# Optimization experiments

Hardware: AMD Instinct MI355X
Metric: run time of the kernel (lower is better)

Reference implementation:

```python
import jax, jax.numpy as jnp
import numpy as np

IN_F, H, T, NUM_CLASSES, WINDOW_HALF = 14, 24, 25, 4, 12


def _lstm_dir(x_tbf, w_ih, w_hh, b_ih, b_hh, reverse):
    # x_tbf: [T,B,F]; w_ih: [4H,F]; w_hh: [4H,H]; biases: [4H]
    B = x_tbf.shape[1]
    xw = jnp.einsum('tbf,gf->tbg', x_tbf, w_ih) + b_ih + b_hh  # [T,B,4H]

    def step(carry, xw_t):
        h, c = carry
        gates = xw_t + h @ w_hh.T
        i, f, g, o = jnp.split(gates, 4, axis=-1)
        i, f, o = jax.nn.sigmoid(i), jax.nn.sigmoid(f), jax.nn.sigmoid(o)
        g = jnp.tanh(g)
        c = f * c + i * g
        h = o * jnp.tanh(c)
        return (h, c), h

    h0 = jnp.zeros((B, H), x_tbf.dtype)
    c0 = jnp.zeros((B, H), x_tbf.dtype)
    _, hs = jax.lax.scan(step, (h0, c0), xw, reverse=reverse)
    return hs  # [T,B,H], in original time order


def setup_inputs() -> dict:
    key = jax.random.key(0)
    ks = jax.random.split(key, 12)
    s_ih = 1.0 / np.sqrt(H)
    u = lambda k, shape: jax.random.uniform(k, shape, jnp.float32, -s_ih, s_ih)
    return {
        'x': jax.random.normal(ks[0], (65536, T, IN_F), jnp.float32),
        'w_ih_f': u(ks[1], (4 * H, IN_F)),
        'w_hh_f': u(ks[2], (4 * H, H)),
        'b_ih_f': u(ks[3], (4 * H,)),
        'b_hh_f': u(ks[4], (4 * H,)),
        'w_ih_b': u(ks[5], (4 * H, IN_F)),
        'w_hh_b': u(ks[6], (4 * H, H)),
        'b_ih_b': u(ks[7], (4 * H,)),
        'b_hh_b': u(ks[8], (4 * H,)),
        'head_w': u(ks[9], (NUM_CLASSES, 2 * H)),
        'head_b': u(ks[10], (NUM_CLASSES,)),
    }


def reference(x, w_ih_f, w_hh_f, b_ih_f, b_hh_f, w_ih_b, w_hh_b, b_ih_b, b_hh_b, head_w, head_b):
    x_tbf = jnp.transpose(x, (1, 0, 2))  # [T,B,F]
    h_f = _lstm_dir(x_tbf, w_ih_f, w_hh_f, b_ih_f, b_hh_f, reverse=False)
    h_b = _lstm_dir(x_tbf, w_ih_b, w_hh_b, b_ih_b, b_hh_b, reverse=True)
    center = jnp.concatenate([h_f[WINDOW_HALF], h_b[WINDOW_HALF]], axis=-1)  # [B,2H]
    # dropout is identity in eval mode
    return center @ head_w.T + head_b  # [B,4]
```

## Files before the change

### kernel.cpp

```cpp
#include <hip/hip_runtime.h>

typedef __attribute__((ext_vector_type(8))) short frag8;
typedef __attribute__((ext_vector_type(4))) float f4;
typedef __attribute__((ext_vector_type(4))) unsigned int u4;
typedef __attribute__((ext_vector_type(2))) float f2;

namespace {
constexpr int T_STEPS = 25;
constexpr int IN_F    = 14;
constexpr int H       = 24;
constexpr int NSTEP   = 13;
constexpr int WAVE_LDS = NSTEP * 1024;
constexpr float LOG2E    = 1.4426950408889634f;
constexpr float TWOLOG2E = 2.8853900817779268f;
}

#if __has_builtin(__builtin_amdgcn_exp2f)
#define EXP2F(v) __builtin_amdgcn_exp2f(v)
#else
#define EXP2F(v) __expf(0.6931471805599453f * (v))
#endif

__device__ __forceinline__ unsigned short bf16_rne(float f) {
    unsigned int u = __float_as_uint(f);
    u += 0x7fff + ((u >> 16) & 1);
    return (unsigned short)(u >> 16);
}
__device__ __forceinline__ float bf16_to_f(unsigned short s) {
    return __uint_as_float(((unsigned int)s) << 16);
}
__device__ __forceinline__ float fast_rcp(float x) { return __builtin_amdgcn_rcpf(x); }

__global__ void pack_mfma(const float* __restrict__ wif, const float* __restrict__ whf,
                          const float* __restrict__ bif, const float* __restrict__ bhf,
                          const float* __restrict__ wib, const float* __restrict__ whb,
                          const float* __restrict__ bib, const float* __restrict__ bhb,
                          unsigned short* __restrict__ ws)
{
    const int gid = blockIdx.x * 256 + threadIdx.x;
    if (gid >= 1536) return;
    const int lane = gid & 63;
    const int tile = (gid >> 6) % 6;
    const int set  = (gid / 384) & 1;
    const int dir  = gid / 768;
    const int m = lane & 15, q = lane >> 4;
    const int g = (tile < 4) ? tile : (m & 3);
    const int u_row = (tile < 4) ? m : ((tile == 4 ? 16 : 20) + (m >> 2));
    const float* Wx = dir ? wib : wif;
    const float* Wh = dir ? whb : whf;
    const float* bi = dir ? bib : bif;
    const float* bh = dir ? bhb : bhf;
    const int rowW = g * 24 + u_row;
    const float scale = (g == 2) ? TWOLOG2E : -LOG2E;
    unsigned short vals[8];
    #pragma unroll
    for (int j = 0; j < 8; ++j) {
        const int k = q * 8 + j;
        unsigned short o = 0;
        if (set == 0) {
            if (k < 28) {
                const int f = (k < 14) ? k : k - 14;
                o = bf16_rne(scale * Wx[rowW * IN_F + f]);
            } else if (k < 30) {
                const float b = scale * (bi[rowW] + bh[rowW]);
                const unsigned short hi = bf16_rne(b);
                o = (k == 28) ? hi : bf16_rne(b - bf16_to_f(hi));
            }
        } else {
            const int j7 = k & 7, kq = k >> 3;
            int uh = -1;
            if (j7 < 4)       uh = kq * 4 + j7;
            else if (j7 == 4) uh = 16 + kq;
            else if (j7 == 5) uh = 20 + kq;
            if (uh >= 0) o = bf16_rne(scale * Wh[rowW * H + uh]);
        }
        vals[j] = o;
    }
    unsigned short* d = ws + (size_t)gid * 8;
    #pragma unroll
    for (int j = 0; j < 8; ++j) d[j] = vals[j];
}

__global__ __launch_bounds__(128, 3)
void bilstm_mfma(const float* __restrict__ x, const unsigned short* __restrict__ wpk,
                 const float* __restrict__ head_w, const float* __restrict__ head_b,
                 float* __restrict__ out, int B)
{
    __align__(16) __shared__ unsigned char arena[2 * WAVE_LDS];

    const int tid  = threadIdx.x;
    const int wave = __builtin_amdgcn_readfirstlane(tid >> 6);
    const int lane = tid & 63;
    const int q    = lane >> 4;
    const int col  = lane & 15;
    const int b0   = blockIdx.x * 16;

    frag8 Aw[2][6];
    #pragma unroll
    for (int s = 0; s < 2; ++s)
        #pragma unroll
        for (int t = 0; t < 6; ++t)
            Aw[s][t] = ((const frag8*)wpk)[((wave * 2 + s) * 6 + t) * 64 + lane];

    unsigned char* xbase = arena + wave * WAVE_LDS;

    auto stage_x = [&](int si, int e) {
        const int t = wave ? (T_STEPS - 1 - si) : si;
        const float* xr = x + ((size_t)(b0 + e) * T_STEPS + t) * IN_F;
        unsigned int xu[IN_F];
        #pragma unroll
        for (int i = 0; i < 7; ++i) {
            f2 v = *(const f2*)(xr + 2 * i);
            xu[2*i] = __float_as_uint(v.x); xu[2*i+1] = __float_as_uint(v.y);
        }
        unsigned int lo[IN_F];
        #pragma unroll
        for (int i = 0; i < IN_F; ++i)
            lo[i] = __float_as_uint(__uint_as_float(xu[i])
                                    - __uint_as_float(xu[i] & 0xFFFF0000u));
        unsigned int w[16];
        #pragma unroll
        for (int i = 0; i < 7; ++i)
            w[i] = __builtin_amdgcn_perm(xu[2*i+1], xu[2*i], 0x07060302u);
        w[7] = __builtin_amdgcn_perm(lo[1], lo[0], 0x07060302u);
        #pragma unroll
        for (int i = 0; i < 6; ++i)
            w[8 + i] = __builtin_amdgcn_perm(lo[2*i+3], lo[2*i+2], 0x07060302u);
        w[14] = 0x3F803F80u;
        w[15] = 0u;
        #pragma unroll
        for (int qq = 0; qq < 4; ++qq)
            *(u4*)(xbase + si * 1024 + qq * 256 + e * 16) =
                (u4){w[qq*4], w[qq*4+1], w[qq*4+2], w[qq*4+3]};
    };

    for (int rr = lane; rr < NSTEP * 16; rr += 64) stage_x(rr >> 4, rr & 15);

    f4    cv = {0.f, 0.f, 0.f, 0.f};
    float c_s[2] = {0.f, 0.f};
    f4    Hv;
    float h_s[2];
    frag8 Bhh, Bhl;
    const f4 zc = {0.f, 0.f, 0.f, 0.f};

    const unsigned char* xrd = xbase + q * 256 + col * 16;

    auto gates = [&](const f4* acc) {
        f4 EI, EF, EG, EO, EC;
        #pragma unroll
        for (int r = 0; r < 4; ++r) {
            EI[r] = EXP2F(acc[0][r]);
            EF[r] = EXP2F(acc[1][r]);
            EG[r] = EXP2F(acc[2][r]);
            EO[r] = EXP2F(acc[3][r]);
        }
        const f4 P  = (EI + 1.0f) * (EG + 1.0f);
        const f4 Df = P * (EF + 1.0f);
        f4 Rf;
        #pragma unroll
        for (int r = 0; r < 4; ++r) Rf[r] = fast_rcp(Df[r]);
        cv = (cv * P + (EG - 1.0f) * (EF + 1.0f)) * Rf;
        #pragma unroll
        for (int r = 0; r < 4; ++r) EC[r] = EXP2F(TWOLOG2E * cv[r]);
        const f4 Do = (EO + 1.0f) * (EC + 1.0f);
        f4 Ro;
        #pragma unroll
        for (int r = 0; r < 4; ++r) Ro[r] = fast_rcp(Do[r]);
        Hv = (EC - 1.0f) * Ro;

        #pragma unroll
        for (int s = 0; s < 2; ++s) {
            const float ei = EXP2F(acc[4 + s][0]);
            const float ef = EXP2F(acc[4 + s][1]);
            const float eg = EXP2F(acc[4 + s][2]);
            const float eo = EXP2F(acc[4 + s][3]);
            const float P2 = (1.0f + ei) * (1.0f + eg);
            const float cn = (c_s[s] * P2 + (eg - 1.0f) * (1.0f + ef))
                             * fast_rcp(P2 * (1.0f + ef));
            c_s[s] = cn;
            const float ec = EXP2F(TWOLOG2E * cn);
            h_s[s] = (ec - 1.0f) * fast_rcp((1.0f + eo) * (1.0f + ec));
        }

        f4 Hl;
        #pragma unroll
        for (int r = 0; r < 4; ++r)
            Hl[r] = Hv[r] - __uint_as_float(__float_as_uint(Hv[r]) & 0xFFFF0000u);
        const float hl4 = h_s[0] - __uint_as_float(__float_as_uint(h_s[0]) & 0xFFFF0000u);
        const float hl5 = h_s[1] - __uint_as_float(__float_as_uint(h_s[1]) & 0xFFFF0000u);
        const u4 uh4 = {
            __builtin_amdgcn_perm(__float_as_uint(Hv[1]), __float_as_uint(Hv[0]), 0x07060302u),
            __builtin_amdgcn_perm(__float_as_uint(Hv[3]), __float_as_uint(Hv[2]), 0x07060302u),
            __builtin_amdgcn_perm(__float_as_uint(h_s[1]), __float_as_uint(h_s[0]), 0x07060302u),
            0u};
        const u4 ul4 = {
            __builtin_amdgcn_perm(__float_as_uint(Hl[1]), __float_as_uint(Hl[0]), 0x07060302u),
            __builtin_amdgcn_perm(__float_as_uint(Hl[3]), __float_as_uint(Hl[2]), 0x07060302u),
            __builtin_amdgcn_perm(__float_as_uint(hl5), __float_as_uint(hl4), 0x07060302u),
            0u};
        Bhh = __builtin_bit_cast(frag8, uh4);
        Bhl = __builtin_bit_cast(frag8, ul4);
    };

    {
        const frag8 Bx = *(const frag8*)(xrd);
        f4 acc[6];
        #pragma unroll
        for (int t = 0; t < 6; ++t)
            acc[t] = __builtin_amdgcn_mfma_f32_16x16x32_bf16(Aw[0][t], Bx, zc, 0, 0, 0);
        gates(acc);
    }

    #pragma unroll 1
    for (int s = 1; s < NSTEP; ++s) {
        const frag8 Bx = *(const frag8*)(xrd + s * 1024);
        f4 acc[6];
        #pragma unroll
        for (int t = 0; t < 6; ++t) {
            acc[t] = __builtin_amdgcn_mfma_f32_16x16x32_bf16(Aw[0][t], Bx,  zc,     0, 0, 0);
            acc[t] = __builtin_amdgcn_mfma_f32_16x16x32_bf16(Aw[1][t], Bhh, acc[t], 0, 0, 0);
            acc[t] = __builtin_amdgcn_mfma_f32_16x16x32_bf16(Aw[1][t], Bhl, acc[t], 0, 0, 0);
        }
        gates(acc);
    }

    *(f4*)(xbase + col * 96 + q * 16) = Hv;
    *(float*)(xbase + col * 96 + 64 + q * 4) = h_s[0];
    *(float*)(xbase + col * 96 + 80 + q * 4) = h_s[1];

    __syncthreads();

    if (tid < 64) {
        const int e = tid >> 2, cls = tid & 3;
        float acc = head_b[cls];
        const float* hf = (const float*)(arena + e * 96);
        const float* hb = (const float*)(arena + WAVE_LDS + e * 96);
        #pragma unroll
        for (int u = 0; u < H; ++u)
            acc += hf[u] * head_w[cls * 2 * H + u] + hb[u] * head_w[cls * 2 * H + H + u];
        out[(size_t)b0 * 4 + tid] = acc;
    }
}

extern "C" void kernel_launch(void* const* d_in, const int* in_sizes, int n_in,
                              void* d_out, int out_size, void* d_ws, size_t ws_size,
                              hipStream_t stream)
{
    const float* x      = (const float*)d_in[0];
    const float* w_ih_f = (const float*)d_in[1];
    const float* w_hh_f = (const float*)d_in[2];
    const float* b_ih_f = (const float*)d_in[3];
    const float* b_hh_f = (const float*)d_in[4];
    const float* w_ih_b = (const float*)d_in[5];
    const float* w_hh_b = (const float*)d_in[6];
    const float* b_ih_b = (const float*)d_in[7];
    const float* b_hh_b = (const float*)d_in[8];
    const float* head_w = (const float*)d_in[9];
    const float* head_b = (const float*)d_in[10];
    float* out = (float*)d_out;
    unsigned short* ws = (unsigned short*)d_ws;

    const int B = in_sizes[0] / (T_STEPS * IN_F);

    hipLaunchKernelGGL(pack_mfma, dim3(6), dim3(256), 0, stream,
                       w_ih_f, w_hh_f, b_ih_f, b_hh_f,
                       w_ih_b, w_hh_b, b_ih_b, b_hh_b, ws);
    hipLaunchKernelGGL(bilstm_mfma, dim3((B + 15) / 16), dim3(128), 0, stream,
                       x, ws, head_w, head_b, out, B);
}
```

Before: 178.7 us.

## Stream x staging in double-buffered 4-step chunks overlapped with recurrence

Replaces the up-front staging of all 13 timesteps of x into LDS with a double-buffered scheme. Each chunk holds 4 steps, and the global loads for the next chunk are issued before computing the current one. LDS per block shrinks from about 26KB to 16KB, and launch bounds rise from 3 to 4 blocks per SIMD for more occupancy. The cost is register pressure from keeping the prefetched values live, plus possible spills under the tighter occupancy bound.

Result: faster. 174.6 us (-2.3%).

```diff
diff --git a/kernel.cpp b/kernel.cpp
--- a/kernel.cpp
+++ b/kernel.cpp
@@ -10,7 +10,8 @@
 constexpr int IN_F    = 14;
 constexpr int H       = 24;
 constexpr int NSTEP   = 13;
-constexpr int WAVE_LDS = NSTEP * 1024;
+constexpr int CHUNK_B  = 4 * 1024;
+constexpr int WAVE_BUF = 2 * CHUNK_B;
 constexpr float LOG2E    = 1.4426950408889634f;
 constexpr float TWOLOG2E = 2.8853900817779268f;
 }
@@ -81,12 +82,12 @@
     for (int j = 0; j < 8; ++j) d[j] = vals[j];
 }
 
-__global__ __launch_bounds__(128, 3)
+__global__ __launch_bounds__(128, 4)
 void bilstm_mfma(const float* __restrict__ x, const unsigned short* __restrict__ wpk,
                  const float* __restrict__ head_w, const float* __restrict__ head_b,
                  float* __restrict__ out, int B)
 {
-    __align__(16) __shared__ unsigned char arena[2 * WAVE_LDS];
+    __align__(16) __shared__ unsigned char arena[2 * WAVE_BUF];
 
     const int tid  = threadIdx.x;
     const int wave = __builtin_amdgcn_readfirstlane(tid >> 6);
@@ -102,17 +103,27 @@
         for (int t = 0; t < 6; ++t)
             Aw[s][t] = ((const frag8*)wpk)[((wave * 2 + s) * 6 + t) * 64 + lane];
 
-    unsigned char* xbase = arena + wave * WAVE_LDS;
-
-    auto stage_x = [&](int si, int e) {
-        const int t = wave ? (T_STEPS - 1 - si) : si;
+    unsigned char* bufA = arena + wave * WAVE_BUF;
+    unsigned char* bufB = bufA + CHUNK_B;
+
+    unsigned int L[IN_F];
+
+    auto stage_load = [&](int c, unsigned int* xu) {
+        const int si = c * 4 + (lane >> 4);
+        const int e  = lane & 15;
+        const int t  = wave ? (T_STEPS - 1 - si) : si;
         const float* xr = x + ((size_t)(b0 + e) * T_STEPS + t) * IN_F;
-        unsigned int xu[IN_F];
         #pragma unroll
         for (int i = 0; i < 7; ++i) {
             f2 v = *(const f2*)(xr + 2 * i);
             xu[2*i] = __float_as_uint(v.x); xu[2*i+1] = __float_as_uint(v.y);
         }
+    };
+
+    auto stage_write = [&](int c, const unsigned int* xu, unsigned char* buf) {
+        if (c == 3 && lane >= 16) return;
+        const int sl = lane >> 4;
+        const int e  = lane & 15;
         unsigned int lo[IN_F];
         #pragma unroll
         for (int i = 0; i < IN_F; ++i)
@@ -130,11 +141,9 @@
         w[15] = 0u;
         #pragma unroll
         for (int qq = 0; qq < 4; ++qq)
-            *(u4*)(xbase + si * 1024 + qq * 256 + e * 16) =
+            *(u4*)(buf + sl * 1024 + qq * 256 + e * 16) =
                 (u4){w[qq*4], w[qq*4+1], w[qq*4+2], w[qq*4+3]};
     };
-
-    for (int rr = lane; rr < NSTEP * 16; rr += 64) stage_x(rr >> 4, rr & 15);
 
     f4    cv = {0.f, 0.f, 0.f, 0.f};
     float c_s[2] = {0.f, 0.f};
@@ -142,8 +151,6 @@
     float h_s[2];
     frag8 Bhh, Bhl;
     const f4 zc = {0.f, 0.f, 0.f, 0.f};
-
-    const unsigned char* xrd = xbase + q * 256 + col * 16;
 
     auto gates = [&](const f4* acc) {
         f4 EI, EF, EG, EO, EC;
@@ -202,18 +209,8 @@
         Bhl = __builtin_bit_cast(frag8, ul4);
     };
 
-    {
-        const frag8 Bx = *(const frag8*)(xrd);
-        f4 acc[6];
-        #pragma unroll
-        for (int t = 0; t < 6; ++t)
-            acc[t] = __builtin_amdgcn_mfma_f32_16x16x32_bf16(Aw[0][t], Bx, zc, 0, 0, 0);
-        gates(acc);
-    }
-
-    #pragma unroll 1
-    for (int s = 1; s < NSTEP; ++s) {
-        const frag8 Bx = *(const frag8*)(xrd + s * 1024);
+    auto full_step = [&](const unsigned char* bp, int r) {
+        const frag8 Bx = *(const frag8*)(bp + r * 1024 + q * 256 + col * 16);
         f4 acc[6];
         #pragma unroll
         for (int t = 0; t < 6; ++t) {
@@ -222,11 +219,40 @@
             acc[t] = __builtin_amdgcn_mfma_f32_16x16x32_bf16(Aw[1][t], Bhl, acc[t], 0, 0, 0);
         }
         gates(acc);
-    }
-
-    *(f4*)(xbase + col * 96 + q * 16) = Hv;
-    *(float*)(xbase + col * 96 + 64 + q * 4) = h_s[0];
-    *(float*)(xbase + col * 96 + 80 + q * 4) = h_s[1];
+    };
+
+    stage_load(0, L);
+    stage_write(0, L, bufA);
+    stage_load(1, L);
+
+    {
+        const frag8 Bx = *(const frag8*)(bufA + q * 256 + col * 16);
+        f4 acc[6];
+        #pragma unroll
+        for (int t = 0; t < 6; ++t)
+            acc[t] = __builtin_amdgcn_mfma_f32_16x16x32_bf16(Aw[0][t], Bx, zc, 0, 0, 0);
+        gates(acc);
+    }
+
+    #pragma unroll 1
+    for (int r = 1; r < 4; ++r) full_step(bufA, r);
+
+    #pragma unroll 1
+    for (int cc = 1; cc <= 2; ++cc) {
+        unsigned char* wb = (cc & 1) ? bufB : bufA;
+        stage_write(cc, L, wb);
+        stage_load(cc + 1, L);
+        #pragma unroll 1
+        for (int r = 0; r < 4; ++r) full_step(wb, r);
+    }
+
+    stage_write(3, L, bufB);
+    full_step(bufB, 0);
+
+    unsigned char* hbase = arena + wave * WAVE_BUF;
+    *(f4*)(hbase + col * 96 + q * 16) = Hv;
+    *(float*)(hbase + col * 96 + 64 + q * 4) = h_s[0];
+    *(float*)(hbase + col * 96 + 80 + q * 4) = h_s[1];
 
     __syncthreads();
 
@@ -234,7 +260,7 @@
         const int e = tid >> 2, cls = tid & 3;
         float acc = head_b[cls];
         const float* hf = (const float*)(arena + e * 96);
-        const float* hb = (const float*)(arena + WAVE_LDS + e * 96);
+        const float* hb = (const float*)(arena + WAVE_BUF + e * 96);
         #pragma unroll
         for (int u = 0; u < H; ++u)
             acc += hf[u] * head_w[cls * 2 * H + u] + hb[u] * head_w[cls * 2 * H + H + u];
```

## Load x directly into MFMA fragments per step, dropping LDS staging

Applied to the files above, without the earlier changes.

Drops the up-front staging of all 13 timesteps of x into LDS. Each lane now loads its own x slice from global memory one step ahead and builds the bf16 hi/lo B fragment in registers, with the weight packing reordered to match the new K layout. The smaller LDS footprint lets launch bounds rise from 3 to 4 blocks per SIMD, raising occupancy. The cost is global load latency inside the serial recurrence, hidden only by a one-step prefetch, plus uncoalesced 8-byte loads.

Measured after the change: 178.3 us. No clear change (-0.2%).

```diff
diff --git a/kernel.cpp b/kernel.cpp
--- a/kernel.cpp
+++ b/kernel.cpp
@@ -10,7 +10,6 @@
 constexpr int IN_F    = 14;
 constexpr int H       = 24;
 constexpr int NSTEP   = 13;
-constexpr int WAVE_LDS = NSTEP * 1024;
 constexpr float LOG2E    = 1.4426950408889634f;
 constexpr float TWOLOG2E = 2.8853900817779268f;
 }
@@ -55,18 +54,22 @@
     unsigned short vals[8];
     #pragma unroll
     for (int j = 0; j < 8; ++j) {
-        const int k = q * 8 + j;
         unsigned short o = 0;
         if (set == 0) {
-            if (k < 28) {
-                const int f = (k < 14) ? k : k - 14;
+            if (q < 3) {
+                const int f = 4 * q + (j & 3);
                 o = bf16_rne(scale * Wx[rowW * IN_F + f]);
-            } else if (k < 30) {
-                const float b = scale * (bi[rowW] + bh[rowW]);
-                const unsigned short hi = bf16_rne(b);
-                o = (k == 28) ? hi : bf16_rne(b - bf16_to_f(hi));
+            } else {
+                if (j == 0 || j == 4)      o = bf16_rne(scale * Wx[rowW * IN_F + 12]);
+                else if (j == 1 || j == 5) o = bf16_rne(scale * Wx[rowW * IN_F + 13]);
+                else if (j == 2 || j == 3) {
+                    const float b = scale * (bi[rowW] + bh[rowW]);
+                    const unsigned short hi = bf16_rne(b);
+                    o = (j == 2) ? hi : bf16_rne(b - bf16_to_f(hi));
+                }
             }
         } else {
+            const int k = q * 8 + j;
             const int j7 = k & 7, kq = k >> 3;
             int uh = -1;
             if (j7 < 4)       uh = kq * 4 + j7;
@@ -81,12 +84,76 @@
     for (int j = 0; j < 8; ++j) d[j] = vals[j];
 }
 
-__global__ __launch_bounds__(128, 3)
+__device__ __forceinline__ void lstm_gates(const f4* acc, f4& cv, float& c_s0, float& c_s1,
+                                           f4& Hv, float& h_s0, float& h_s1,
+                                           frag8& Bhh, frag8& Bhl)
+{
+    f4 EI, EF, EG, EO, EC;
+    #pragma unroll
+    for (int r = 0; r < 4; ++r) {
+        EI[r] = EXP2F(acc[0][r]);
+        EF[r] = EXP2F(acc[1][r]);
+        EG[r] = EXP2F(acc[2][r]);
+        EO[r] = EXP2F(acc[3][r]);
+    }
+    const f4 P  = (EI + 1.0f) * (EG + 1.0f);
+    const f4 Df = P * (EF + 1.0f);
+    f4 Rf;
+    #pragma unroll
+    for (int r = 0; r < 4; ++r) Rf[r] = fast_rcp(Df[r]);
+    cv = (cv * P + (EG - 1.0f) * (EF + 1.0f)) * Rf;
+    #pragma unroll
+    for (int r = 0; r < 4; ++r) EC[r] = EXP2F(TWOLOG2E * cv[r]);
+    const f4 Do = (EO + 1.0f) * (EC + 1.0f);
+    f4 Ro;
+    #pragma unroll
+    for (int r = 0; r < 4; ++r) Ro[r] = fast_rcp(Do[r]);
+    Hv = (EC - 1.0f) * Ro;
+
+    float hs[2];
+    float cs[2] = {c_s0, c_s1};
+    #pragma unroll
+    for (int s = 0; s < 2; ++s) {
+        const float ei = EXP2F(acc[4 + s][0]);
+        const float ef = EXP2F(acc[4 + s][1]);
+        const float eg = EXP2F(acc[4 + s][2]);
+        const float eo = EXP2F(acc[4 + s][3]);
+        const float P2 = (1.0f + ei) * (1.0f + eg);
+        const float cn = (cs[s] * P2 + (eg - 1.0f) * (1.0f + ef))
+                         * fast_rcp(P2 * (1.0f + ef));
+        cs[s] = cn;
+        const float ec = EXP2F(TWOLOG2E * cn);
+        hs[s] = (ec - 1.0f) * fast_rcp((1.0f + eo) * (1.0f + ec));
+    }
+    c_s0 = cs[0]; c_s1 = cs[1];
+    h_s0 = hs[0]; h_s1 = hs[1];
+
+    f4 Hl;
+    #pragma unroll
+    for (int r = 0; r < 4; ++r)
+        Hl[r] = Hv[r] - __uint_as_float(__float_as_uint(Hv[r]) & 0xFFFF0000u);
+    const float hl4 = hs[0] - __uint_as_float(__float_as_uint(hs[0]) & 0xFFFF0000u);
+    const float hl5 = hs[1] - __uint_as_float(__float_as_uint(hs[1]) & 0xFFFF0000u);
+    const u4 uh4 = {
+        __builtin_amdgcn_perm(__float_as_uint(Hv[1]), __float_as_uint(Hv[0]), 0x07060302u),
+        __builtin_amdgcn_perm(__float_as_uint(Hv[3]), __float_as_uint(Hv[2]), 0x07060302u),
+        __builtin_amdgcn_perm(__float_as_uint(hs[1]), __float_as_uint(hs[0]), 0x07060302u),
+        0u};
+    const u4 ul4 = {
+        __builtin_amdgcn_perm(__float_as_uint(Hl[1]), __float_as_uint(Hl[0]), 0x07060302u),
+        __builtin_amdgcn_perm(__float_as_uint(Hl[3]), __float_as_uint(Hl[2]), 0x07060302u),
+        __builtin_amdgcn_perm(__float_as_uint(hl5), __float_as_uint(hl4), 0x07060302u),
+        0u};
+    Bhh = __builtin_bit_cast(frag8, uh4);
+    Bhl = __builtin_bit_cast(frag8, ul4);
+}
+
+__global__ __launch_bounds__(128, 4)
 void bilstm_mfma(const float* __restrict__ x, const unsigned short* __restrict__ wpk,
                  const float* __restrict__ head_w, const float* __restrict__ head_b,
                  float* __restrict__ out, int B)
 {
-    __align__(16) __shared__ unsigned char arena[2 * WAVE_LDS];
+    __align__(16) __shared__ unsigned char arena[2 * 1536];
 
     const int tid  = threadIdx.x;
     const int wave = __builtin_amdgcn_readfirstlane(tid >> 6);
@@ -102,118 +169,56 @@
         for (int t = 0; t < 6; ++t)
             Aw[s][t] = ((const frag8*)wpk)[((wave * 2 + s) * 6 + t) * 64 + lane];
 
-    unsigned char* xbase = arena + wave * WAVE_LDS;
-
-    auto stage_x = [&](int si, int e) {
-        const int t = wave ? (T_STEPS - 1 - si) : si;
-        const float* xr = x + ((size_t)(b0 + e) * T_STEPS + t) * IN_F;
-        unsigned int xu[IN_F];
-        #pragma unroll
-        for (int i = 0; i < 7; ++i) {
-            f2 v = *(const f2*)(xr + 2 * i);
-            xu[2*i] = __float_as_uint(v.x); xu[2*i+1] = __float_as_uint(v.y);
-        }
-        unsigned int lo[IN_F];
-        #pragma unroll
-        for (int i = 0; i < IN_F; ++i)
-            lo[i] = __float_as_uint(__uint_as_float(xu[i])
-                                    - __uint_as_float(xu[i] & 0xFFFF0000u));
-        unsigned int w[16];
-        #pragma unroll
-        for (int i = 0; i < 7; ++i)
-            w[i] = __builtin_amdgcn_perm(xu[2*i+1], xu[2*i], 0x07060302u);
-        w[7] = __builtin_amdgcn_perm(lo[1], lo[0], 0x07060302u);
-        #pragma unroll
-        for (int i = 0; i < 6; ++i)
-            w[8 + i] = __builtin_amdgcn_perm(lo[2*i+3], lo[2*i+2], 0x07060302u);
-        w[14] = 0x3F803F80u;
-        w[15] = 0u;
-        #pragma unroll
-        for (int qq = 0; qq < 4; ++qq)
-            *(u4*)(xbase + si * 1024 + qq * 256 + e * 16) =
-                (u4){w[qq*4], w[qq*4+1], w[qq*4+2], w[qq*4+3]};
+    const bool q3 = (q == 3);
+    const unsigned int biasor = q3 ? 0x3F803F80u : 0u;
+    const int  boff  = q3 ? 40 : q * 16;
+    const int  t0    = wave ? (T_STEPS - 1) : 0;
+    const int  dstep = wave ? -(IN_F * 4) : (IN_F * 4);
+    const char* px = (const char*)x
+                   + ((size_t)(b0 + col) * T_STEPS + t0) * (IN_F * 4) + boff;
+
+    auto build_bx = [&](f2 la, f2 lb) -> frag8 {
+        const float a0 = q3 ? lb.x : la.x;
+        const float a1 = q3 ? lb.y : la.y;
+        const float a2 = q3 ? 0.0f : lb.x;
+        const float a3 = q3 ? 0.0f : lb.y;
+        const float l0 = a0 - __uint_as_float(__float_as_uint(a0) & 0xFFFF0000u);
+        const float l1 = a1 - __uint_as_float(__float_as_uint(a1) & 0xFFFF0000u);
+        const float l2 = a2 - __uint_as_float(__float_as_uint(a2) & 0xFFFF0000u);
+        const float l3 = a3 - __uint_as_float(__float_as_uint(a3) & 0xFFFF0000u);
+        const u4 w = {
+            __builtin_amdgcn_perm(__float_as_uint(a1), __float_as_uint(a0), 0x07060302u),
+            __builtin_amdgcn_perm(__float_as_uint(a3), __float_as_uint(a2), 0x07060302u) | biasor,
+            __builtin_amdgcn_perm(__float_as_uint(l1), __float_as_uint(l0), 0x07060302u),
+            __builtin_amdgcn_perm(__float_as_uint(l3), __float_as_uint(l2), 0x07060302u)};
+        return __builtin_bit_cast(frag8, w);
     };
 
-    for (int rr = lane; rr < NSTEP * 16; rr += 64) stage_x(rr >> 4, rr & 15);
-
     f4    cv = {0.f, 0.f, 0.f, 0.f};
-    float c_s[2] = {0.f, 0.f};
+    float c_s0 = 0.f, c_s1 = 0.f;
     f4    Hv;
-    float h_s[2];
+    float h_s0, h_s1;
     frag8 Bhh, Bhl;
     const f4 zc = {0.f, 0.f, 0.f, 0.f};
 
-    const unsigned char* xrd = xbase + q * 256 + col * 16;
-
-    auto gates = [&](const f4* acc) {
-        f4 EI, EF, EG, EO, EC;
-        #pragma unroll
-        for (int r = 0; r < 4; ++r) {
-            EI[r] = EXP2F(acc[0][r]);
-            EF[r] = EXP2F(acc[1][r]);
-            EG[r] = EXP2F(acc[2][r]);
-            EO[r] = EXP2F(acc[3][r]);
-        }
-        const f4 P  = (EI + 1.0f) * (EG + 1.0f);
-        const f4 Df = P * (EF + 1.0f);
-        f4 Rf;
-        #pragma unroll
-        for (int r = 0; r < 4; ++r) Rf[r] = fast_rcp(Df[r]);
-        cv = (cv * P + (EG - 1.0f) * (EF + 1.0f)) * Rf;
-        #pragma unroll
-        for (int r = 0; r < 4; ++r) EC[r] = EXP2F(TWOLOG2E * cv[r]);
-        const f4 Do = (EO + 1.0f) * (EC + 1.0f);
-        f4 Ro;
-        #pragma unroll
-        for (int r = 0; r < 4; ++r) Ro[r] = fast_rcp(Do[r]);
-        Hv = (EC - 1.0f) * Ro;
-
-        #pragma unroll
-        for (int s = 0; s < 2; ++s) {
-            const float ei = EXP2F(acc[4 + s][0]);
-            const float ef = EXP2F(acc[4 + s][1]);
-            const float eg = EXP2F(acc[4 + s][2]);
-            const float eo = EXP2F(acc[4 + s][3]);
-            const float P2 = (1.0f + ei) * (1.0f + eg);
-            const float cn = (c_s[s] * P2 + (eg - 1.0f) * (1.0f + ef))
-                             * fast_rcp(P2 * (1.0f + ef));
-            c_s[s] = cn;
-            const float ec = EXP2F(TWOLOG2E * cn);
-            h_s[s] = (ec - 1.0f) * fast_rcp((1.0f + eo) * (1.0f + ec));
-        }
-
-        f4 Hl;
-        #pragma unroll
-        for (int r = 0; r < 4; ++r)
-            Hl[r] = Hv[r] - __uint_as_float(__float_as_uint(Hv[r]) & 0xFFFF0000u);
-        const float hl4 = h_s[0] - __uint_as_float(__float_as_uint(h_s[0]) & 0xFFFF0000u);
-        const float hl5 = h_s[1] - __uint_as_float(__float_as_uint(h_s[1]) & 0xFFFF0000u);
-        const u4 uh4 = {
-            __builtin_amdgcn_perm(__float_as_uint(Hv[1]), __float_as_uint(Hv[0]), 0x07060302u),
-            __builtin_amdgcn_perm(__float_as_uint(Hv[3]), __float_as_uint(Hv[2]), 0x07060302u),
-            __builtin_amdgcn_perm(__float_as_uint(h_s[1]), __float_as_uint(h_s[0]), 0x07060302u),
-            0u};
-        const u4 ul4 = {
-            __builtin_amdgcn_perm(__float_as_uint(Hl[1]), __float_as_uint(Hl[0]), 0x07060302u),
-            __builtin_amdgcn_perm(__float_as_uint(Hl[3]), __float_as_uint(Hl[2]), 0x07060302u),
-            __builtin_amdgcn_perm(__float_as_uint(hl5), __float_as_uint(hl4), 0x07060302u),
-            0u};
-        Bhh = __builtin_bit_cast(frag8, uh4);
-        Bhl = __builtin_bit_cast(frag8, ul4);
-    };
+    f2 la = *(const f2*)px;
+    f2 lb = *(const f2*)(px + 8);
+    px += dstep;
 
     {
-        const frag8 Bx = *(const frag8*)(xrd);
+        const frag8 Bx = build_bx(la, lb);
+        la = *(const f2*)px; lb = *(const f2*)(px + 8); px += dstep;
         f4 acc[6];
         #pragma unroll
         for (int t = 0; t < 6; ++t)
             acc[t] = __builtin_amdgcn_mfma_f32_16x16x32_bf16(Aw[0][t], Bx, zc, 0, 0, 0);
-        gates(acc);
+        lstm_gates(acc, cv, c_s0, c_s1, Hv, h_s0, h_s1, Bhh, Bhl);
     }
 
     #pragma unroll 1
     for (int s = 1; s < NSTEP; ++s) {
-        const frag8 Bx = *(const frag8*)(xrd + s * 1024);
+        const frag8 Bx = build_bx(la, lb);
+        la = *(const f2*)px; lb = *(const f2*)(px + 8); px += dstep;
         f4 acc[6];
         #pragma unroll
         for (int t = 0; t < 6; ++t) {
@@ -221,12 +226,13 @@
             acc[t] = __builtin_amdgcn_mfma_f32_16x16x32_bf16(Aw[1][t], Bhh, acc[t], 0, 0, 0);
             acc[t] = __builtin_amdgcn_mfma_f32_16x16x32_bf16(Aw[1][t], Bhl, acc[t], 0, 0, 0);
         }
-        gates(acc);
-    }
-
-    *(f4*)(xbase + col * 96 + q * 16) = Hv;
-    *(float*)(xbase + col * 96 + 64 + q * 4) = h_s[0];
-    *(float*)(xbase + col * 96 + 80 + q * 4) = h_s[1];
+        lstm_gates(acc, cv, c_s0, c_s1, Hv, h_s0, h_s1, Bhh, Bhl);
+    }
+
+    unsigned char* hbase = arena + wave * 1536;
+    *(f4*)(hbase + col * 96 + q * 16) = Hv;
+    *(float*)(hbase + col * 96 + 64 + q * 4) = h_s0;
+    *(float*)(hbase + col * 96 + 80 + q * 4) = h_s1;
 
     __syncthreads();
 
@@ -234,7 +240,7 @@
         const int e = tid >> 2, cls = tid & 3;
         float acc = head_b[cls];
         const float* hf = (const float*)(arena + e * 96);
-        const float* hb = (const float*)(arena + WAVE_LDS + e * 96);
+        const float* hb = (const float*)(arena + 1536 + e * 96);
         #pragma unroll
         for (int u = 0; u < H; ++u)
             acc += hf[u] * head_w[cls * 2 * H + u] + hb[u] * head_w[cls * 2 * H + H + u];
```
